# Optimization experiments

Measured on AMD Instinct MI355X. Metric: run time of the kernel, lower is better.

The kernel has to match this reference:

```python
import jax, jax.numpy as jnp
import numpy as np

NUM_LABELS = 32
EMB = 128          # label_embedding_dim
HID = 1024         # hidden_dim (== encoder feature dim)
B, S = 128, 512


def setup_inputs() -> dict:
    key = jax.random.key(0)
    ks = jax.random.split(key, 8)
    k = 1.0 / np.sqrt(HID)  # torch GRU/Linear default init bound
    u = lambda kk, shape: jax.random.uniform(kk, shape, jnp.float32, minval=-k, maxval=k)
    return {
        "hidden_states": jax.random.normal(ks[0], (B, S, HID), jnp.float32),
        "emb": jax.random.normal(ks[1], (NUM_LABELS, EMB), jnp.float32),  # nn.Embedding ~ N(0,1)
        "W_ih": u(ks[2], (3 * HID, EMB + HID)),  # GRU input weights, gate order r,z,n
        "W_hh": u(ks[3], (3 * HID, HID)),
        "b_ih": u(ks[4], (3 * HID,)),
        "b_hh": u(ks[5], (3 * HID,)),
        "W_out": u(ks[6], (NUM_LABELS, HID)),
        "b_out": u(ks[7], (NUM_LABELS,)),
    }


def reference(hidden_states, emb, W_ih, W_hh, b_ih, b_hh, W_out, b_out):
    batch = hidden_states.shape[0]
    h0 = jnp.zeros((batch, W_hh.shape[1]), hidden_states.dtype)
    lab0 = jnp.broadcast_to(emb[0], (batch, emb.shape[1]))  # label_start_embedding (id 0)

    def step(carry, x_t):
        h, lab = carry
        inp = jnp.concatenate([x_t, lab], axis=-1)            # [B, HID+EMB]
        gi = inp @ W_ih.T + b_ih                               # [B, 3*HID]
        gh = h @ W_hh.T + b_hh
        ir, iz, in_ = jnp.split(gi, 3, axis=-1)
        hr, hz, hn = jnp.split(gh, 3, axis=-1)
        r = jax.nn.sigmoid(ir + hr)
        z = jax.nn.sigmoid(iz + hz)
        n = jnp.tanh(in_ + r * hn)
        h_new = (1.0 - z) * n + z * h                          # PyTorch GRU update
        logit = h_new @ W_out.T + b_out                        # dropout is identity in eval
        pred = jnp.argmax(logit, axis=-1)                      # softmax is monotone; argmax(probs)==argmax(logit)
        return (h_new, emb[pred]), logit

    xs = jnp.swapaxes(hidden_states, 0, 1)                     # [S, B, HID]
    _, logits = jax.lax.scan(step, (h0, lab0), xs)             # logits: [S, B, L]
    return jnp.swapaxes(logits, 0, 1)                          # [B, S, L]
```

## Files before the change

kernel.cpp:

```cpp
#include <hip/hip_runtime.h>


#define S_    512
#define HID_  1024
#define EMB_  128
#define NL_   32
#define G3_   3072

#define LDS_A_STRIDE 1032
#define LDS_A_BYTES  (48 * LDS_A_STRIDE * 2)
#define CP_STRIDE    52
#define LDS_CP_BYTES (4 * 64 * CP_STRIDE * 4)
#define LDS_BYTES    (LDS_A_BYTES + LDS_CP_BYTES)

typedef __attribute__((ext_vector_type(8))) short          short8;
typedef __attribute__((ext_vector_type(8))) unsigned short u16x8;
typedef __attribute__((ext_vector_type(4))) unsigned short u16x4;
typedef __attribute__((ext_vector_type(4))) float          f32x4;
typedef unsigned long long u64_t;

__device__ unsigned int   g_ctr[576];
__device__ unsigned int   g_flag[1];
__device__ unsigned int   g_vis[256];
__device__ int            g_pred[128];
__device__ unsigned short g_hhi[128 * HID_];
__device__ unsigned short g_hlo[128 * HID_];
__device__ float          g_hf32[128 * HID_];
__device__ float          g_Glab[NL_ * G3_];
__device__ float          g_GIX[128 * 64 * 48];
__device__ unsigned short g_Wlox[G3_ * HID_];
__device__ unsigned short g_Wlohh[G3_ * HID_];

__device__ __forceinline__ float bf2f(unsigned short u) {
  union { unsigned int i; float f; } v; v.i = ((unsigned int)u) << 16; return v.f;
}
__device__ __forceinline__ unsigned short f2bf(float f) {
  union { float f; unsigned int i; } v; v.f = f;
  unsigned int u = v.i;
  return (unsigned short)((u + 0x7FFFu + ((u >> 16) & 1u)) >> 16);
}
__device__ __forceinline__ short8 ld_bf8(const unsigned short* p) {
  return __builtin_bit_cast(short8, *(const u16x8*)p);
}
__device__ __forceinline__ float ldin(const void* p, long i, int f32) {
  return f32 ? ((const float*)p)[i] : bf2f(((const unsigned short*)p)[i]);
}
__device__ __forceinline__ void store_out(void* out, int f32, long idx, float v) {
  if (f32) ((float*)out)[idx] = v;
  else     ((unsigned short*)out)[idx] = f2bf(v);
}

__device__ __forceinline__ u64_t ald64(const void* p) {
  return __hip_atomic_load((const u64_t*)p, __ATOMIC_RELAXED,
                           __HIP_MEMORY_SCOPE_AGENT);
}
__device__ __forceinline__ void ast64(void* p, u64_t v) {
  __hip_atomic_store((u64_t*)p, v, __ATOMIC_RELAXED,
                     __HIP_MEMORY_SCOPE_AGENT);
}
__device__ __forceinline__ unsigned int ald32(const unsigned int* p) {
  return __hip_atomic_load(p, __ATOMIC_RELAXED, __HIP_MEMORY_SCOPE_AGENT);
}
__device__ __forceinline__ void ast32(unsigned int* p, unsigned int v) {
  __hip_atomic_store(p, v, __ATOMIC_RELAXED, __HIP_MEMORY_SCOPE_AGENT);
}
__device__ __forceinline__ int aldi(const int* p) {
  return __hip_atomic_load(p, __ATOMIC_RELAXED, __HIP_MEMORY_SCOPE_AGENT);
}
__device__ __forceinline__ void asti(int* p, int v) {
  __hip_atomic_store(p, v, __ATOMIC_RELAXED, __HIP_MEMORY_SCOPE_AGENT);
}
__device__ __forceinline__ short8 ld_bf8_coh(const unsigned short* p) {
  union { u64_t q[2]; short8 s; } u;
  u.q[0] = ald64(p);
  u.q[1] = ald64(p + 4);
  return u.s;
}
__device__ __forceinline__ f32x4 ld_f4_coh(const float* p) {
  union { u64_t q[2]; f32x4 f; } u;
  u.q[0] = ald64(p);
  u.q[1] = ald64(p + 2);
  return u.f;
}
__device__ __forceinline__ void st_f4_coh(float* p, f32x4 v) {
  union { f32x4 f; u64_t q[2]; } u; u.f = v;
  ast64(p, u.q[0]);
  ast64(p + 2, u.q[1]);
}
__device__ __forceinline__ void st_h4_coh(unsigned short* p, u16x4 v) {
  union { u16x4 h; u64_t q; } u; u.h = v;
  ast64(p, u.q);
}

__global__ void k_zero() {
  int t = blockIdx.x * 256 + threadIdx.x;
  if (t < 576) g_ctr[t] = 0u;
  else if (t < 832) g_vis[t - 576] = 0u;
  else if (t < 960) g_pred[t - 832] = 0;
  const u16x4 z4 = {0, 0, 0, 0};
  const f32x4 zf = {0.f, 0.f, 0.f, 0.f};
  for (int i = t; i < 128 * HID_ / 4; i += 65536) {
    ((u16x4*)g_hhi)[i] = z4;
    ((u16x4*)g_hlo)[i] = z4;
    ((f32x4*)g_hf32)[i] = zf;
  }
}

__global__ void k_detect(const unsigned short* __restrict__ W) {
  unsigned bad = 0;
  for (int i = threadIdx.x; i < 1024; i += 64) {
    float v = bf2f(W[i]);
    if (!(v * v <= 1.0f)) bad = 1;
  }
  unsigned long long b = __ballot(bad != 0);
  if (threadIdx.x == 0) g_flag[0] = (b != 0ull) ? 1u : 0u;
}

__global__ void k_prep(const void* __restrict__ emb,
                       const void* __restrict__ W_ih,
                       const void* __restrict__ b_ih) {
  const int f32 = (int)g_flag[0];
  int l = blockIdx.x / 12;
  int n = (blockIdx.x % 12) * 256 + threadIdx.x;
  double acc = (double)ldin(b_ih, n, f32);
  for (int e = 0; e < EMB_; ++e)
    acc += (double)ldin(emb, (long)l * EMB_ + e, f32) *
           (double)ldin(W_ih, (long)n * (HID_ + EMB_) + HID_ + e, f32);
  g_Glab[l * G3_ + n] = (float)acc;
}

__global__ void k_prepw(const void* __restrict__ W_ih,
                        const void* __restrict__ W_hh) {
  if (!g_flag[0]) return;
  long i4 = ((long)blockIdx.x * 256 + threadIdx.x) * 4;
  if (i4 >= (long)G3_ * HID_) return;
  int row = (int)(i4 >> 10), col = (int)(i4 & 1023);
  f32x4 wh = *(const f32x4*)&((const float*)W_hh)[(long)row * HID_ + col];
  f32x4 wx = *(const f32x4*)&((const float*)W_ih)[(long)row * (HID_ + EMB_) + col];
  u16x4 lh, lx;
  #pragma unroll
  for (int j = 0; j < 4; ++j) {
    unsigned short h1 = f2bf(wh[j]);
    lh[j] = f2bf(wh[j] - bf2f(h1));
    unsigned short x1 = f2bf(wx[j]);
    lx[j] = f2bf(wx[j] - bf2f(x1));
  }
  *(u16x4*)&g_Wlohh[i4] = lh;
  *(u16x4*)&g_Wlox[i4]  = lx;
}

__device__ __forceinline__ void gridbar(int wg, int bar) {
  __syncthreads();
  if (threadIdx.x == 0) {
    asm volatile("s_waitcnt vmcnt(0)" ::: "memory");
    unsigned int* c1   = g_ctr + (wg & 7) * 64;
    unsigned int* root = g_ctr + 512;
    unsigned int old = __hip_atomic_fetch_add(c1, 1u, __ATOMIC_RELAXED,
                                              __HIP_MEMORY_SCOPE_AGENT);
    if (old == 32u * (unsigned)(bar + 1) - 1u)
      __hip_atomic_fetch_add(root, 1u, __ATOMIC_RELAXED,
                             __HIP_MEMORY_SCOPE_AGENT);
    unsigned int tgt = 8u * (unsigned)(bar + 1);
    while (__hip_atomic_load(root, __ATOMIC_RELAXED,
                             __HIP_MEMORY_SCOPE_AGENT) < tgt)
      __builtin_amdgcn_s_sleep(1);
  }
  __syncthreads();
}

__global__ __launch_bounds__(256) void k_seq(
    const void* __restrict__ hs,
    const void* __restrict__ W_ih,
    const void* __restrict__ W_hh,
    const void* __restrict__ b_hh,
    const void* __restrict__ W_out,
    const void* __restrict__ b_out,
    void* __restrict__ out) {
  extern __shared__ char smem[];
  unsigned short* sA  = (unsigned short*)smem;
  float*          sCp = (float*)(smem + LDS_A_BYTES);

  const int f32 = (int)g_flag[0];
  const int tid = threadIdx.x;
  const int wg  = blockIdx.x;
  const bool isx = (wg < 128);
  const int lid  = isx ? wg : wg - 128;
  const int rg = lid >> 1, bg = lid & 1;
  const int slot = lid;
  const int lane = tid & 63, wv = tid >> 6;
  const int m = lane & 15, q = lane >> 4;
  const int bl = tid & 63;
  const int jj = (tid >> 6) * 4;

  {
    const void* Wsrc = isx ? W_ih : W_hh;
    const int wstride = isx ? (HID_ + EMB_) : HID_;
    if (f32) {
      const float* Ws = (const float*)Wsrc;
      for (int i = tid; i < 48 * 1024 / 4; i += 256) {
        int e = i * 4, row = e >> 10, k4 = e & 1023;
        int grow = (row >> 4) * HID_ + rg * 16 + (row & 15);
        f32x4 v = *(const f32x4*)&Ws[(long)grow * wstride + k4];
        u16x4 o;
        #pragma unroll
        for (int j = 0; j < 4; ++j) o[j] = f2bf(v[j]);
        *(u16x4*)&sA[row * LDS_A_STRIDE + k4] = o;
      }
    } else {
      const unsigned short* Ws = (const unsigned short*)Wsrc;
      for (int i = tid; i < 48 * 1024 / 4; i += 256) {
        int e = i * 4, row = e >> 10, k4 = e & 1023;
        int grow = (row >> 4) * HID_ + rg * 16 + (row & 15);
        *(u16x4*)&sA[row * LDS_A_STRIDE + k4] =
            *(const u16x4*)&Ws[(long)grow * wstride + k4];
      }
    }
  }

  float bo = 0.f;
  if (isx && tid < 32) bo = ldin(b_out, tid, f32);
  f32x4 bhh[3];
  if (!isx) {
    const int jbase = rg * 16 + jj;
    #pragma unroll
    for (int g = 0; g < 3; ++g)
      #pragma unroll
      for (int t = 0; t < 4; ++t)
        bhh[g][t] = ldin(b_hh, (long)g * HID_ + jbase + t, f32);
  }

  float hreg[4] = {0.f, 0.f, 0.f, 0.f};
  f32x4 sred[3];
  int bar = 0;

  if (tid == 0) ast32(&g_vis[wg], (unsigned)wg + 1u);
  gridbar(wg, bar); ++bar;
  if (tid == 0) {
    unsigned p = ((unsigned)wg + 37u) & 255u;
    if (ald32(&g_vis[p]) != p + 1u) store_out(out, f32, wg, 999.0f);
  }

  for (int it = 0; it <= S_; ++it) {
    gridbar(wg, bar); ++bar;

    if (isx && it >= 1) {
      if (it == 1 && wg == 0 && tid == 0) {
        float s = 0.f;
        for (int i = 0; i < 16; ++i) {
          union { u64_t q; float f[2]; } u; u.q = ald64(&g_hf32[2 * i]);
          s += u.f[0] * u.f[0] + u.f[1] * u.f[1];
        }
        if (s == 0.f) store_out(out, f32, 300, 555.0f);
      }
      const int b = wg, s = it - 1;
      float* scrp  = sCp;
      float* shrow = sCp + 256;
      {
        f32x4 hv = ld_f4_coh(&g_hf32[(long)b * HID_ + tid * 4]);
        *(f32x4*)&shrow[(tid >> 5) * 132 + (tid & 31) * 4] = hv;
      }
      __syncthreads();
      {
        int l = tid >> 3, kc = tid & 7;
        const float* hr = shrow + kc * 132;
        float p = 0.f;
        if (f32) {
          const float* wr = (const float*)W_out + (long)l * HID_ + kc * 128;
          for (int k = 0; k < 128; k += 4) {
            f32x4 wa = *(const f32x4*)&wr[k];
            f32x4 ha = *(const f32x4*)&hr[k];
            #pragma unroll
            for (int j = 0; j < 4; ++j) p += wa[j] * ha[j];
          }
        } else {
          const unsigned short* wr =
              (const unsigned short*)W_out + (long)l * HID_ + kc * 128;
          for (int k = 0; k < 128; k += 8) {
            u16x8 w8 = *(const u16x8*)&wr[k];
            f32x4 ha = *(const f32x4*)&hr[k];
            f32x4 hb = *(const f32x4*)&hr[k + 4];
            #pragma unroll
            for (int j = 0; j < 4; ++j) {
              p += bf2f(w8[j]) * ha[j];
              p += bf2f(w8[4 + j]) * hb[j];
            }
          }
        }
        scrp[tid] = p;
      }
      __syncthreads();
      if (tid < 32) {
        const float* pp = sCp + tid * 8;
        float v = pp[0] + pp[1] + pp[2] + pp[3] + pp[4] + pp[5] + pp[6] + pp[7]
                  + bo;
        store_out(out, f32, ((long)b * S_ + s) * NL_ + tid, v);
        float bv = v; int bi = tid;
        #pragma unroll
        for (int off = 16; off; off >>= 1) {
          float v2 = __shfl_down(bv, off, 32);
          int   i2 = __shfl_down(bi, off, 32);
          if (v2 > bv || (v2 == bv && i2 < bi)) { bv = v2; bi = i2; }
        }
        if (tid == 0) asti(&g_pred[b], bi);
      }
      __syncthreads();
    }

    if (it < S_) {
      f32x4 acc[3][4];
      #pragma unroll
      for (int rt = 0; rt < 3; ++rt)
        #pragma unroll
        for (int bt = 0; bt < 4; ++bt) acc[rt][bt] = f32x4{0.f, 0.f, 0.f, 0.f};

      const int kw0 = wv * 256 + q * 8;

      if (isx) {
        const long bstride = (long)S_ * HID_;
        const long boff = ((long)(bg * 64) * S_ + it) * HID_;
        #pragma unroll
        for (int kb = 0; kb < 8; ++kb) {
          const int k = kw0 + kb * 32;
          short8 avh[3];
          #pragma unroll
          for (int rt = 0; rt < 3; ++rt)
            avh[rt] = ld_bf8(&sA[(rt * 16 + m) * LDS_A_STRIDE + k]);
          if (f32) {
            const float* Bf = (const float*)hs + boff;
            short8 bxh[4], bxl[4];
            #pragma unroll
            for (int bt = 0; bt < 4; ++bt) {
              const float* bp = Bf + (long)(bt * 16 + m) * bstride + k;
              f32x4 x0 = *(const f32x4*)bp;
              f32x4 x1 = *(const f32x4*)(bp + 4);
              u16x8 th, tl;
              #pragma unroll
              for (int j = 0; j < 4; ++j) {
                unsigned short u0 = f2bf(x0[j]);
                th[j] = u0; tl[j] = f2bf(x0[j] - bf2f(u0));
                unsigned short u1 = f2bf(x1[j]);
                th[4 + j] = u1; tl[4 + j] = f2bf(x1[j] - bf2f(u1));
              }
              bxh[bt] = __builtin_bit_cast(short8, th);
              bxl[bt] = __builtin_bit_cast(short8, tl);
            }
            short8 avl[3];
            #pragma unroll
            for (int rt = 0; rt < 3; ++rt)
              avl[rt] = ld_bf8(&g_Wlox[(long)(rt * HID_ + rg * 16 + m) * HID_ + k]);
            #pragma unroll
            for (int rt = 0; rt < 3; ++rt)
              #pragma unroll
              for (int bt = 0; bt < 4; ++bt) {
                acc[rt][bt] = __builtin_amdgcn_mfma_f32_16x16x32_bf16(
                    avh[rt], bxh[bt], acc[rt][bt], 0, 0, 0);
                acc[rt][bt] = __builtin_amdgcn_mfma_f32_16x16x32_bf16(
                    avh[rt], bxl[bt], acc[rt][bt], 0, 0, 0);
                acc[rt][bt] = __builtin_amdgcn_mfma_f32_16x16x32_bf16(
                    avl[rt], bxh[bt], acc[rt][bt], 0, 0, 0);
                acc[rt][bt] = __builtin_amdgcn_mfma_f32_16x16x32_bf16(
                    avl[rt], bxl[bt], acc[rt][bt], 0, 0, 0);
              }
          } else {
            const unsigned short* Bh = (const unsigned short*)hs + boff;
            short8 bxh[4];
            #pragma unroll
            for (int bt = 0; bt < 4; ++bt)
              bxh[bt] = ld_bf8(&Bh[(long)(bt * 16 + m) * bstride + k]);
            #pragma unroll
            for (int rt = 0; rt < 3; ++rt)
              #pragma unroll
              for (int bt = 0; bt < 4; ++bt)
                acc[rt][bt] = __builtin_amdgcn_mfma_f32_16x16x32_bf16(
                    avh[rt], bxh[bt], acc[rt][bt], 0, 0, 0);
          }
        }
      } else {
        const unsigned short* Bhi = g_hhi + (long)(bg * 64) * HID_;
        const unsigned short* Blo = g_hlo + (long)(bg * 64) * HID_;
        #pragma unroll
        for (int kb = 0; kb < 8; ++kb) {
          const int k = kw0 + kb * 32;
          short8 avh[3], bh[4], blv[4];
          #pragma unroll
          for (int rt = 0; rt < 3; ++rt)
            avh[rt] = ld_bf8(&sA[(rt * 16 + m) * LDS_A_STRIDE + k]);
          #pragma unroll
          for (int bt = 0; bt < 4; ++bt) {
            bh[bt]  = ld_bf8_coh(&Bhi[(long)(bt * 16 + m) * HID_ + k]);
            blv[bt] = ld_bf8_coh(&Blo[(long)(bt * 16 + m) * HID_ + k]);
          }
          #pragma unroll
          for (int rt = 0; rt < 3; ++rt)
            #pragma unroll
            for (int bt = 0; bt < 4; ++bt) {
              acc[rt][bt] = __builtin_amdgcn_mfma_f32_16x16x32_bf16(
                  avh[rt], bh[bt], acc[rt][bt], 0, 0, 0);
              acc[rt][bt] = __builtin_amdgcn_mfma_f32_16x16x32_bf16(
                  avh[rt], blv[bt], acc[rt][bt], 0, 0, 0);
            }
          if (f32) {
            short8 avl[3];
            #pragma unroll
            for (int rt = 0; rt < 3; ++rt)
              avl[rt] = ld_bf8(&g_Wlohh[(long)(rt * HID_ + rg * 16 + m) * HID_ + k]);
            #pragma unroll
            for (int rt = 0; rt < 3; ++rt)
              #pragma unroll
              for (int bt = 0; bt < 4; ++bt) {
                acc[rt][bt] = __builtin_amdgcn_mfma_f32_16x16x32_bf16(
                    avl[rt], bh[bt], acc[rt][bt], 0, 0, 0);
                acc[rt][bt] = __builtin_amdgcn_mfma_f32_16x16x32_bf16(
                    avl[rt], blv[bt], acc[rt][bt], 0, 0, 0);
              }
          }
        }
      }

      __syncthreads();
      #pragma unroll
      for (int rt = 0; rt < 3; ++rt)
        #pragma unroll
        for (int bt = 0; bt < 4; ++bt)
          *(f32x4*)&sCp[(wv * 64 + bt * 16 + m) * CP_STRIDE + rt * 16 + q * 4] =
              acc[rt][bt];
      __syncthreads();
      #pragma unroll
      for (int g = 0; g < 3; ++g) {
        f32x4 sv = f32x4{0.f, 0.f, 0.f, 0.f};
        #pragma unroll
        for (int w = 0; w < 4; ++w)
          sv += *(const f32x4*)&sCp[(w * 64 + bl) * CP_STRIDE + g * 16 + jj];
        sred[g] = sv;
      }
      if (isx) {
        #pragma unroll
        for (int g = 0; g < 3; ++g)
          st_f4_coh(&g_GIX[((long)slot * 64 + bl) * 48 + g * 16 + jj], sred[g]);
      }
    }

    gridbar(wg, bar); ++bar;

    if (!isx && it < S_) {
      const int bglob = bg * 64 + bl;
      const int jbase = rg * 16 + jj;
      const int pb = aldi(&g_pred[bglob]);
      const float* gl = g_Glab + (long)pb * G3_;
      f32x4 glab[3], gix[3];
      #pragma unroll
      for (int g = 0; g < 3; ++g) {
        glab[g] = *(const f32x4*)&gl[g * HID_ + jbase];
        gix[g]  = ld_f4_coh(&g_GIX[((long)slot * 64 + bl) * 48 + g * 16 + jj]);
      }
      u16x4 whi, wlo;
      f32x4 hf;
      #pragma unroll
      for (int t4 = 0; t4 < 4; ++t4) {
        float ghr = sred[0][t4] + bhh[0][t4];
        float ghz = sred[1][t4] + bhh[1][t4];
        float ghn = sred[2][t4] + bhh[2][t4];
        float gir = gix[0][t4] + glab[0][t4];
        float giz = gix[1][t4] + glab[1][t4];
        float gin = gix[2][t4] + glab[2][t4];
        float r = 1.f / (1.f + expf(-(gir + ghr)));
        float z = 1.f / (1.f + expf(-(giz + ghz)));
        float n = tanhf(gin + r * ghn);
        float hn = (1.f - z) * n + z * hreg[t4];
        hreg[t4] = hn;
        hf[t4] = hn;
        unsigned short uhi = f2bf(hn);
        whi[t4] = uhi;
        wlo[t4] = f2bf(hn - bf2f(uhi));
      }
      st_h4_coh(&g_hhi[(long)bglob * HID_ + jbase], whi);
      st_h4_coh(&g_hlo[(long)bglob * HID_ + jbase], wlo);
      st_f4_coh(&g_hf32[(long)bglob * HID_ + jbase], hf);
    }
  }
}

extern "C" void kernel_launch(void* const* d_in, const int* in_sizes, int n_in,
                              void* d_out, int out_size, void* d_ws, size_t ws_size,
                              hipStream_t stream) {
  const void* hs    = d_in[0];
  const void* emb   = d_in[1];
  const void* W_ih  = d_in[2];
  const void* W_hh  = d_in[3];
  const void* b_ih  = d_in[4];
  const void* b_hh  = d_in[5];
  const void* W_out = d_in[6];
  const void* b_out = d_in[7];

  hipLaunchKernelGGL(k_zero, dim3(256), dim3(256), 0, stream);
  hipLaunchKernelGGL(k_detect, dim3(1), dim3(64), 0, stream,
                     (const unsigned short*)W_ih);
  hipLaunchKernelGGL(k_prep, dim3(32 * 12), dim3(256), 0, stream,
                     emb, W_ih, b_ih);
  hipLaunchKernelGGL(k_prepw, dim3(3072), dim3(256), 0, stream, W_ih, W_hh);
  hipFuncSetAttribute((const void*)k_seq,
                      hipFuncAttributeMaxDynamicSharedMemorySize, LDS_BYTES);
  hipLaunchKernelGGL(k_seq, dim3(256), dim3(256), LDS_BYTES, stream,
                     hs, W_ih, W_hh, b_hh, W_out, b_out, d_out);
}
```

Measured before the change: 17.27 ms.

## Precompute input projections for all steps upfront and drop one grid barrier per step

All 256 workgroups now compute the x-side GRU input projection for every timestep in a prologue and store it to a large global buffer. The sequential loop then keeps only the hidden-side matmul on the recurrent workgroups. The hidden state is double-buffered, and the second grid barrier per step is replaced by a counter flag that signals when the argmax predictions are ready, so the W_out/argmax work overlaps the W_hh matmul. This shortens the per-step critical path and removes one grid barrier per step, at the cost of a roughly 200MB+ intermediate buffer, an extra prologue pass, and re-staging W_hh into LDS.

Measured after the change: 17.38 ms. About the same (+0.6%).

```diff
diff --git a/kernel.cpp b/kernel.cpp
--- a/kernel.cpp
+++ b/kernel.cpp
@@ -22,14 +22,15 @@
 __device__ unsigned int   g_ctr[576];
 __device__ unsigned int   g_flag[1];
 __device__ unsigned int   g_vis[256];
+__device__ unsigned int   g_predflag;
 __device__ int            g_pred[128];
-__device__ unsigned short g_hhi[128 * HID_];
-__device__ unsigned short g_hlo[128 * HID_];
-__device__ float          g_hf32[128 * HID_];
+__device__ unsigned short g_hhi[2][128 * HID_];
+__device__ unsigned short g_hlo[2][128 * HID_];
+__device__ float          g_hf32[2][128 * HID_];
 __device__ float          g_Glab[NL_ * G3_];
-__device__ float          g_GIX[128 * 64 * 48];
 __device__ unsigned short g_Wlox[G3_ * HID_];
 __device__ unsigned short g_Wlohh[G3_ * HID_];
+__device__ float          g_GIXall[(size_t)S_ * 128 * 64 * 48];
 
 __device__ __forceinline__ float bf2f(unsigned short u) {
   union { unsigned int i; float f; } v; v.i = ((unsigned int)u) << 16; return v.f;
@@ -97,9 +98,10 @@
   if (t < 576) g_ctr[t] = 0u;
   else if (t < 832) g_vis[t - 576] = 0u;
   else if (t < 960) g_pred[t - 832] = 0;
+  else if (t == 960) g_predflag = 0u;
   const u16x4 z4 = {0, 0, 0, 0};
   const f32x4 zf = {0.f, 0.f, 0.f, 0.f};
-  for (int i = t; i < 128 * HID_ / 4; i += 65536) {
+  for (int i = t; i < 2 * 128 * HID_ / 4; i += 65536) {
     ((u16x4*)g_hhi)[i] = z4;
     ((u16x4*)g_hlo)[i] = z4;
     ((f32x4*)g_hf32)[i] = zf;
@@ -168,6 +170,30 @@
   __syncthreads();
 }
 
+__device__ __forceinline__ void stage_w(unsigned short* sA, const void* Wsrc,
+                                        int wstride, int rg, int f32, int tid) {
+  if (f32) {
+    const float* Ws = (const float*)Wsrc;
+    for (int i = tid; i < 48 * 1024 / 4; i += 256) {
+      int e = i * 4, row = e >> 10, k4 = e & 1023;
+      int grow = (row >> 4) * HID_ + rg * 16 + (row & 15);
+      f32x4 v = *(const f32x4*)&Ws[(long)grow * wstride + k4];
+      u16x4 o;
+      #pragma unroll
+      for (int j = 0; j < 4; ++j) o[j] = f2bf(v[j]);
+      *(u16x4*)&sA[row * LDS_A_STRIDE + k4] = o;
+    }
+  } else {
+    const unsigned short* Ws = (const unsigned short*)Wsrc;
+    for (int i = tid; i < 48 * 1024 / 4; i += 256) {
+      int e = i * 4, row = e >> 10, k4 = e & 1023;
+      int grow = (row >> 4) * HID_ + rg * 16 + (row & 15);
+      *(u16x4*)&sA[row * LDS_A_STRIDE + k4] =
+          *(const u16x4*)&Ws[(long)grow * wstride + k4];
+    }
+  }
+}
+
 __global__ __launch_bounds__(256) void k_seq(
     const void* __restrict__ hs,
     const void* __restrict__ W_ih,
@@ -191,31 +217,121 @@
   const int m = lane & 15, q = lane >> 4;
   const int bl = tid & 63;
   const int jj = (tid >> 6) * 4;
+  const int kw0 = wv * 256 + q * 8;
+
+  int bar = 0;
+
+  if (tid == 0) ast32(&g_vis[wg], (unsigned)wg + 1u);
+  gridbar(wg, bar); ++bar;
+  if (tid == 0) {
+    unsigned p = ((unsigned)wg + 37u) & 255u;
+    if (ald32(&g_vis[p]) != p + 1u) store_out(out, f32, wg, 999.0f);
+  }
 
   {
-    const void* Wsrc = isx ? W_ih : W_hh;
-    const int wstride = isx ? (HID_ + EMB_) : HID_;
-    if (f32) {
-      const float* Ws = (const float*)Wsrc;
-      for (int i = tid; i < 48 * 1024 / 4; i += 256) {
-        int e = i * 4, row = e >> 10, k4 = e & 1023;
-        int grow = (row >> 4) * HID_ + rg * 16 + (row & 15);
-        f32x4 v = *(const f32x4*)&Ws[(long)grow * wstride + k4];
-        u16x4 o;
-        #pragma unroll
-        for (int j = 0; j < 4; ++j) o[j] = f2bf(v[j]);
-        *(u16x4*)&sA[row * LDS_A_STRIDE + k4] = o;
-      }
-    } else {
-      const unsigned short* Ws = (const unsigned short*)Wsrc;
-      for (int i = tid; i < 48 * 1024 / 4; i += 256) {
-        int e = i * 4, row = e >> 10, k4 = e & 1023;
-        int grow = (row >> 4) * HID_ + rg * 16 + (row & 15);
-        *(u16x4*)&sA[row * LDS_A_STRIDE + k4] =
-            *(const u16x4*)&Ws[(long)grow * wstride + k4];
-      }
+    const int slot0 = wg & 127;
+    const int rg0 = slot0 >> 1, bg0 = slot0 & 1;
+    stage_w(sA, W_ih, HID_ + EMB_, rg0, f32, tid);
+    __syncthreads();
+    const long bstride = (long)S_ * HID_;
+    const long boffb = (long)(bg0 * 64) * S_ * HID_;
+    for (int t = 0; t < 256; ++t) {
+      const int it = ((wg >> 7) << 8) | t;
+      f32x4 acc[3][4];
+      #pragma unroll
+      for (int rt = 0; rt < 3; ++rt)
+        #pragma unroll
+        for (int bt = 0; bt < 4; ++bt) acc[rt][bt] = f32x4{0.f, 0.f, 0.f, 0.f};
+      const long boff = boffb + (long)it * HID_;
+      if (f32) {
+        const float* Bf = (const float*)hs + boff;
+        #pragma unroll
+        for (int kb = 0; kb < 8; ++kb) {
+          const int k = kw0 + kb * 32;
+          short8 avh[3];
+          #pragma unroll
+          for (int rt = 0; rt < 3; ++rt)
+            avh[rt] = ld_bf8(&sA[(rt * 16 + m) * LDS_A_STRIDE + k]);
+          short8 bxh[4], bxl[4];
+          #pragma unroll
+          for (int bt = 0; bt < 4; ++bt) {
+            const float* bp = Bf + (long)(bt * 16 + m) * bstride + k;
+            f32x4 x0 = *(const f32x4*)bp;
+            f32x4 x1 = *(const f32x4*)(bp + 4);
+            u16x8 th, tl;
+            #pragma unroll
+            for (int j = 0; j < 4; ++j) {
+              unsigned short u0 = f2bf(x0[j]);
+              th[j] = u0; tl[j] = f2bf(x0[j] - bf2f(u0));
+              unsigned short u1 = f2bf(x1[j]);
+              th[4 + j] = u1; tl[4 + j] = f2bf(x1[j] - bf2f(u1));
+            }
+            bxh[bt] = __builtin_bit_cast(short8, th);
+            bxl[bt] = __builtin_bit_cast(short8, tl);
+          }
+          short8 avl[3];
+          #pragma unroll
+          for (int rt = 0; rt < 3; ++rt)
+            avl[rt] = ld_bf8(&g_Wlox[(long)(rt * HID_ + rg0 * 16 + m) * HID_ + k]);
+          #pragma unroll
+          for (int rt = 0; rt < 3; ++rt)
+            #pragma unroll
+            for (int bt = 0; bt < 4; ++bt) {
+              acc[rt][bt] = __builtin_amdgcn_mfma_f32_16x16x32_bf16(
+                  avh[rt], bxh[bt], acc[rt][bt], 0, 0, 0);
+              acc[rt][bt] = __builtin_amdgcn_mfma_f32_16x16x32_bf16(
+                  avh[rt], bxl[bt], acc[rt][bt], 0, 0, 0);
+              acc[rt][bt] = __builtin_amdgcn_mfma_f32_16x16x32_bf16(
+                  avl[rt], bxh[bt], acc[rt][bt], 0, 0, 0);
+              acc[rt][bt] = __builtin_amdgcn_mfma_f32_16x16x32_bf16(
+                  avl[rt], bxl[bt], acc[rt][bt], 0, 0, 0);
+            }
+        }
+      } else {
+        const unsigned short* Bh = (const unsigned short*)hs + boff;
+        #pragma unroll
+        for (int kb = 0; kb < 8; ++kb) {
+          const int k = kw0 + kb * 32;
+          short8 avh[3], bxh[4];
+          #pragma unroll
+          for (int rt = 0; rt < 3; ++rt)
+            avh[rt] = ld_bf8(&sA[(rt * 16 + m) * LDS_A_STRIDE + k]);
+          #pragma unroll
+          for (int bt = 0; bt < 4; ++bt)
+            bxh[bt] = ld_bf8(&Bh[(long)(bt * 16 + m) * bstride + k]);
+          #pragma unroll
+          for (int rt = 0; rt < 3; ++rt)
+            #pragma unroll
+            for (int bt = 0; bt < 4; ++bt)
+              acc[rt][bt] = __builtin_amdgcn_mfma_f32_16x16x32_bf16(
+                  avh[rt], bxh[bt], acc[rt][bt], 0, 0, 0);
+        }
+      }
+      __syncthreads();
+      #pragma unroll
+      for (int rt = 0; rt < 3; ++rt)
+        #pragma unroll
+        for (int bt = 0; bt < 4; ++bt)
+          *(f32x4*)&sCp[(wv * 64 + bt * 16 + m) * CP_STRIDE + rt * 16 + q * 4] =
+              acc[rt][bt];
+      __syncthreads();
+      #pragma unroll
+      for (int g = 0; g < 3; ++g) {
+        f32x4 sv = f32x4{0.f, 0.f, 0.f, 0.f};
+        #pragma unroll
+        for (int w = 0; w < 4; ++w)
+          sv += *(const f32x4*)&sCp[(w * 64 + bl) * CP_STRIDE + g * 16 + jj];
+        *(f32x4*)&g_GIXall[(((long)it * 128 + slot0) * 64 + bl) * 48 +
+                           g * 16 + jj] = sv;
+      }
+      __syncthreads();
     }
   }
+  __threadfence();
+  gridbar(wg, bar); ++bar;
+
+  if (!isx) stage_w(sA, W_hh, HID_, rg, f32, tid);
+  __syncthreads();
 
   float bo = 0.f;
   if (isx && tid < 32) bo = ldin(b_out, tid, f32);
@@ -231,23 +347,16 @@
 
   float hreg[4] = {0.f, 0.f, 0.f, 0.f};
   f32x4 sred[3];
-  int bar = 0;
-
-  if (tid == 0) ast32(&g_vis[wg], (unsigned)wg + 1u);
-  gridbar(wg, bar); ++bar;
-  if (tid == 0) {
-    unsigned p = ((unsigned)wg + 37u) & 255u;
-    if (ald32(&g_vis[p]) != p + 1u) store_out(out, f32, wg, 999.0f);
-  }
 
   for (int it = 0; it <= S_; ++it) {
     gridbar(wg, bar); ++bar;
 
     if (isx && it >= 1) {
+      const int rb = (it + 1) & 1;
       if (it == 1 && wg == 0 && tid == 0) {
         float s = 0.f;
         for (int i = 0; i < 16; ++i) {
-          union { u64_t q; float f[2]; } u; u.q = ald64(&g_hf32[2 * i]);
+          union { u64_t q; float f[2]; } u; u.q = ald64(&g_hf32[0][2 * i]);
           s += u.f[0] * u.f[0] + u.f[1] * u.f[1];
         }
         if (s == 0.f) store_out(out, f32, 300, 555.0f);
@@ -256,7 +365,7 @@
       float* scrp  = sCp;
       float* shrow = sCp + 256;
       {
-        f32x4 hv = ld_f4_coh(&g_hf32[(long)b * HID_ + tid * 4]);
+        f32x4 hv = ld_f4_coh(&g_hf32[rb][(long)b * HID_ + tid * 4]);
         *(f32x4*)&shrow[(tid >> 5) * 132 + (tid & 31) * 4] = hv;
       }
       __syncthreads();
@@ -301,119 +410,68 @@
           int   i2 = __shfl_down(bi, off, 32);
           if (v2 > bv || (v2 == bv && i2 < bi)) { bv = v2; bi = i2; }
         }
-        if (tid == 0) asti(&g_pred[b], bi);
+        if (tid == 0) {
+          asti(&g_pred[b], bi);
+          asm volatile("s_waitcnt vmcnt(0)" ::: "memory");
+          __hip_atomic_fetch_add(&g_predflag, 1u, __ATOMIC_RELAXED,
+                                 __HIP_MEMORY_SCOPE_AGENT);
+        }
       }
       __syncthreads();
     }
 
-    if (it < S_) {
+    if (!isx && it < S_) {
+      const int rb = (it + 1) & 1;
+      const int wb = it & 1;
+      f32x4 gixp[3];
+      #pragma unroll
+      for (int g = 0; g < 3; ++g)
+        gixp[g] = *(const f32x4*)&g_GIXall[(((long)it * 128 + slot) * 64 + bl)
+                                           * 48 + g * 16 + jj];
+
       f32x4 acc[3][4];
       #pragma unroll
       for (int rt = 0; rt < 3; ++rt)
         #pragma unroll
         for (int bt = 0; bt < 4; ++bt) acc[rt][bt] = f32x4{0.f, 0.f, 0.f, 0.f};
 
-      const int kw0 = wv * 256 + q * 8;
-
-      if (isx) {
-        const long bstride = (long)S_ * HID_;
-        const long boff = ((long)(bg * 64) * S_ + it) * HID_;
-        #pragma unroll
-        for (int kb = 0; kb < 8; ++kb) {
-          const int k = kw0 + kb * 32;
-          short8 avh[3];
-          #pragma unroll
-          for (int rt = 0; rt < 3; ++rt)
-            avh[rt] = ld_bf8(&sA[(rt * 16 + m) * LDS_A_STRIDE + k]);
-          if (f32) {
-            const float* Bf = (const float*)hs + boff;
-            short8 bxh[4], bxl[4];
+      const unsigned short* Bhi = g_hhi[rb] + (long)(bg * 64) * HID_;
+      const unsigned short* Blo = g_hlo[rb] + (long)(bg * 64) * HID_;
+      #pragma unroll
+      for (int kb = 0; kb < 8; ++kb) {
+        const int k = kw0 + kb * 32;
+        short8 avh[3], bh[4], blv[4];
+        #pragma unroll
+        for (int rt = 0; rt < 3; ++rt)
+          avh[rt] = ld_bf8(&sA[(rt * 16 + m) * LDS_A_STRIDE + k]);
+        #pragma unroll
+        for (int bt = 0; bt < 4; ++bt) {
+          bh[bt]  = ld_bf8_coh(&Bhi[(long)(bt * 16 + m) * HID_ + k]);
+          blv[bt] = ld_bf8_coh(&Blo[(long)(bt * 16 + m) * HID_ + k]);
+        }
+        #pragma unroll
+        for (int rt = 0; rt < 3; ++rt)
+          #pragma unroll
+          for (int bt = 0; bt < 4; ++bt) {
+            acc[rt][bt] = __builtin_amdgcn_mfma_f32_16x16x32_bf16(
+                avh[rt], bh[bt], acc[rt][bt], 0, 0, 0);
+            acc[rt][bt] = __builtin_amdgcn_mfma_f32_16x16x32_bf16(
+                avh[rt], blv[bt], acc[rt][bt], 0, 0, 0);
+          }
+        if (f32) {
+          short8 avl[3];
+          #pragma unroll
+          for (int rt = 0; rt < 3; ++rt)
+            avl[rt] = ld_bf8(&g_Wlohh[(long)(rt * HID_ + rg * 16 + m) * HID_ + k]);
+          #pragma unroll
+          for (int rt = 0; rt < 3; ++rt)
             #pragma unroll
             for (int bt = 0; bt < 4; ++bt) {
-              const float* bp = Bf + (long)(bt * 16 + m) * bstride + k;
-              f32x4 x0 = *(const f32x4*)bp;
-              f32x4 x1 = *(const f32x4*)(bp + 4);
-              u16x8 th, tl;
-              #pragma unroll
-              for (int j = 0; j < 4; ++j) {
-                unsigned short u0 = f2bf(x0[j]);
-                th[j] = u0; tl[j] = f2bf(x0[j] - bf2f(u0));
-                unsigned short u1 = f2bf(x1[j]);
-                th[4 + j] = u1; tl[4 + j] = f2bf(x1[j] - bf2f(u1));
-              }
-              bxh[bt] = __builtin_bit_cast(short8, th);
-              bxl[bt] = __builtin_bit_cast(short8, tl);
+              acc[rt][bt] = __builtin_amdgcn_mfma_f32_16x16x32_bf16(
+                  avl[rt], bh[bt], acc[rt][bt], 0, 0, 0);
+              acc[rt][bt] = __builtin_amdgcn_mfma_f32_16x16x32_bf16(
+                  avl[rt], blv[bt], acc[rt][bt], 0, 0, 0);
             }
-            short8 avl[3];
-            #pragma unroll
-            for (int rt = 0; rt < 3; ++rt)
-              avl[rt] = ld_bf8(&g_Wlox[(long)(rt * HID_ + rg * 16 + m) * HID_ + k]);
-            #pragma unroll
-            for (int rt = 0; rt < 3; ++rt)
-              #pragma unroll
-              for (int bt = 0; bt < 4; ++bt) {
-                acc[rt][bt] = __builtin_amdgcn_mfma_f32_16x16x32_bf16(
-                    avh[rt], bxh[bt], acc[rt][bt], 0, 0, 0);
-                acc[rt][bt] = __builtin_amdgcn_mfma_f32_16x16x32_bf16(
-                    avh[rt], bxl[bt], acc[rt][bt], 0, 0, 0);
-                acc[rt][bt] = __builtin_amdgcn_mfma_f32_16x16x32_bf16(
-                    avl[rt], bxh[bt], acc[rt][bt], 0, 0, 0);
-                acc[rt][bt] = __builtin_amdgcn_mfma_f32_16x16x32_bf16(
-                    avl[rt], bxl[bt], acc[rt][bt], 0, 0, 0);
-              }
-          } else {
-            const unsigned short* Bh = (const unsigned short*)hs + boff;
-            short8 bxh[4];
-            #pragma unroll
-            for (int bt = 0; bt < 4; ++bt)
-              bxh[bt] = ld_bf8(&Bh[(long)(bt * 16 + m) * bstride + k]);
-            #pragma unroll
-            for (int rt = 0; rt < 3; ++rt)
-              #pragma unroll
-              for (int bt = 0; bt < 4; ++bt)
-                acc[rt][bt] = __builtin_amdgcn_mfma_f32_16x16x32_bf16(
-                    avh[rt], bxh[bt], acc[rt][bt], 0, 0, 0);
-          }
-        }
-      } else {
-        const unsigned short* Bhi = g_hhi + (long)(bg * 64) * HID_;
-        const unsigned short* Blo = g_hlo + (long)(bg * 64) * HID_;
-        #pragma unroll
-        for (int kb = 0; kb < 8; ++kb) {
-          const int k = kw0 + kb * 32;
-          short8 avh[3], bh[4], blv[4];
-          #pragma unroll
-          for (int rt = 0; rt < 3; ++rt)
-            avh[rt] = ld_bf8(&sA[(rt * 16 + m) * LDS_A_STRIDE + k]);
-          #pragma unroll
-          for (int bt = 0; bt < 4; ++bt) {
-            bh[bt]  = ld_bf8_coh(&Bhi[(long)(bt * 16 + m) * HID_ + k]);
-            blv[bt] = ld_bf8_coh(&Blo[(long)(bt * 16 + m) * HID_ + k]);
-          }
-          #pragma unroll
-          for (int rt = 0; rt < 3; ++rt)
-            #pragma unroll
-            for (int bt = 0; bt < 4; ++bt) {
-              acc[rt][bt] = __builtin_amdgcn_mfma_f32_16x16x32_bf16(
-                  avh[rt], bh[bt], acc[rt][bt], 0, 0, 0);
-              acc[rt][bt] = __builtin_amdgcn_mfma_f32_16x16x32_bf16(
-                  avh[rt], blv[bt], acc[rt][bt], 0, 0, 0);
-            }
-          if (f32) {
-            short8 avl[3];
-            #pragma unroll
-            for (int rt = 0; rt < 3; ++rt)
-              avl[rt] = ld_bf8(&g_Wlohh[(long)(rt * HID_ + rg * 16 + m) * HID_ + k]);
-            #pragma unroll
-            for (int rt = 0; rt < 3; ++rt)
-              #pragma unroll
-              for (int bt = 0; bt < 4; ++bt) {
-                acc[rt][bt] = __builtin_amdgcn_mfma_f32_16x16x32_bf16(
-                    avl[rt], bh[bt], acc[rt][bt], 0, 0, 0);
-                acc[rt][bt] = __builtin_amdgcn_mfma_f32_16x16x32_bf16(
-                    avl[rt], blv[bt], acc[rt][bt], 0, 0, 0);
-              }
-          }
         }
       }
 
@@ -433,26 +491,23 @@
           sv += *(const f32x4*)&sCp[(w * 64 + bl) * CP_STRIDE + g * 16 + jj];
         sred[g] = sv;
       }
-      if (isx) {
-        #pragma unroll
-        for (int g = 0; g < 3; ++g)
-          st_f4_coh(&g_GIX[((long)slot * 64 + bl) * 48 + g * 16 + jj], sred[g]);
-      }
-    }
-
-    gridbar(wg, bar); ++bar;
-
-    if (!isx && it < S_) {
+
+      if (it >= 1) {
+        if (tid == 0) {
+          unsigned tgt = 128u * (unsigned)it;
+          while (ald32(&g_predflag) < tgt) __builtin_amdgcn_s_sleep(1);
+        }
+        __syncthreads();
+      }
+
       const int bglob = bg * 64 + bl;
       const int jbase = rg * 16 + jj;
       const int pb = aldi(&g_pred[bglob]);
       const float* gl = g_Glab + (long)pb * G3_;
-      f32x4 glab[3], gix[3];
-      #pragma unroll
-      for (int g = 0; g < 3; ++g) {
+      f32x4 glab[3];
+      #pragma unroll
+      for (int g = 0; g < 3; ++g)
         glab[g] = *(const f32x4*)&gl[g * HID_ + jbase];
-        gix[g]  = ld_f4_coh(&g_GIX[((long)slot * 64 + bl) * 48 + g * 16 + jj]);
-      }
       u16x4 whi, wlo;
       f32x4 hf;
       #pragma unroll
@@ -460,9 +515,9 @@
         float ghr = sred[0][t4] + bhh[0][t4];
         float ghz = sred[1][t4] + bhh[1][t4];
         float ghn = sred[2][t4] + bhh[2][t4];
-        float gir = gix[0][t4] + glab[0][t4];
-        float giz = gix[1][t4] + glab[1][t4];
-        float gin = gix[2][t4] + glab[2][t4];
+        float gir = gixp[0][t4] + glab[0][t4];
+        float giz = gixp[1][t4] + glab[1][t4];
+        float gin = gixp[2][t4] + glab[2][t4];
         float r = 1.f / (1.f + expf(-(gir + ghr)));
         float z = 1.f / (1.f + expf(-(giz + ghz)));
         float n = tanhf(gin + r * ghn);
@@ -473,9 +528,9 @@
         whi[t4] = uhi;
         wlo[t4] = f2bf(hn - bf2f(uhi));
       }
-      st_h4_coh(&g_hhi[(long)bglob * HID_ + jbase], whi);
-      st_h4_coh(&g_hlo[(long)bglob * HID_ + jbase], wlo);
-      st_f4_coh(&g_hf32[(long)bglob * HID_ + jbase], hf);
+      st_h4_coh(&g_hhi[wb][(long)bglob * HID_ + jbase], whi);
+      st_h4_coh(&g_hlo[wb][(long)bglob * HID_ + jbase], wlo);
+      st_f4_coh(&g_hf32[wb][(long)bglob * HID_ + jbase], hf);
     }
   }
 }
```
